# Performance work log

Measured on AMD Instinct MI355X. Metric: run time of the kernel, lower is better.

The kernel has to match this reference:

```python
import jax, jax.numpy as jnp
import numpy as np

B, N, E, I, H = 8, 20000, 320000, 32, 64


def setup_inputs() -> dict:
    key = jax.random.key(0)
    ks = jax.random.split(key, 12)
    s = 0.05
    return {
        "x": jax.random.normal(ks[0], (B, I), jnp.float32),
        "h_prev": jax.random.normal(ks[1], (B, N, H), jnp.float32),
        "src": jax.random.randint(ks[2], (E,), 0, N, jnp.int32),
        "dst": jax.random.randint(ks[3], (E,), 0, N, jnp.int32),
        "w_r_w": jax.random.normal(ks[4], (I, H), jnp.float32) * s,
        "w_r_b": jnp.zeros((H,), jnp.float32),
        "w_z_w": jax.random.normal(ks[5], (I, H), jnp.float32) * s,
        "w_z_b": jnp.zeros((H,), jnp.float32),
        "w_h_w": jax.random.normal(ks[6], (I, H), jnp.float32) * s,
        "w_h_b": jnp.zeros((H,), jnp.float32),
        "gcn_w": jax.random.normal(ks[7], (H, H), jnp.float32) * s,
        "gcn_b": jnp.zeros((H,), jnp.float32),
    }


def _graph_conv(h, src, dst, gcn_w, gcn_b):
    # DGL GraphConv, norm='both': rst = D_in^{-1/2} A (D_out^{-1/2} (H W)) + b
    num_nodes = h.shape[1]
    ones = jnp.ones((src.shape[0],), h.dtype)
    out_deg = jax.ops.segment_sum(ones, src, num_segments=num_nodes)
    in_deg = jax.ops.segment_sum(ones, dst, num_segments=num_nodes)
    out_norm = jax.lax.rsqrt(jnp.clip(out_deg, 1.0))  # [N]
    in_norm = jax.lax.rsqrt(jnp.clip(in_deg, 1.0))    # [N]
    hw = jnp.einsum('bnh,hk->nbk', h, gcn_w)           # [N,B,H] node-major
    feat = hw * out_norm[:, None, None]
    msgs = feat[src]                                   # [E,B,H] gather
    agg = jax.ops.segment_sum(msgs, dst, num_segments=num_nodes)  # [N,B,H]
    agg = agg * in_norm[:, None, None]
    return jnp.swapaxes(agg, 0, 1) + gcn_b             # [B,N,H]


def reference(x, h_prev, src, dst, w_r_w, w_r_b, w_z_w, w_z_b, w_h_w, w_h_b,
              gcn_w, gcn_b):
    # gcn_h is the same module applied to the same h_prev three times in the
    # original -> compute the aggregation once (identical math).
    a = _graph_conv(h_prev, src, dst, gcn_w, gcn_b)    # [B,N,H]
    xr = (x @ w_r_w + w_r_b)[:, None, :]               # [B,1,H] broadcast over nodes
    xz = (x @ w_z_w + w_z_b)[:, None, :]
    xh = (x @ w_h_w + w_h_b)[:, None, :]
    r_t = jax.nn.sigmoid(xr + a)
    z_t = jax.nn.sigmoid(xz + a)
    h_tilde = jnp.tanh(xh + r_t * a)
    h_t = (1.0 - z_t) * h_prev + z_t * h_tilde
    return h_t
```

## Files before the change

kernel.cpp:

```cpp
#include <hip/hip_runtime.h>
#include <hip/hip_bf16.h>
#include <cstdint>

constexpr int B = 8;
constexpr int N = 20000;
constexpr int E = 320000;
constexpr int I = 32;
constexpr int H = 64;
constexpr int BH = B * H;
constexpr int CAP = 64;
constexpr int PAD = 32;

constexpr int GCN_BLOCKS  = 1250;
constexpr int SCAT_BLOCKS = E / 256;

typedef short short8 __attribute__((ext_vector_type(8)));
typedef float f32x4 __attribute__((ext_vector_type(4)));
typedef float f32x2 __attribute__((ext_vector_type(2)));

__device__ __forceinline__ float bf2f(unsigned short u) {
    union { unsigned int i; float f; } c;
    c.i = ((unsigned int)u) << 16;
    return c.f;
}
__device__ __forceinline__ unsigned short f2bf(float f) {
    unsigned int u = __float_as_uint(f);
    u += 0x7fffu + ((u >> 16) & 1u);
    return (unsigned short)(u >> 16);
}
__device__ __forceinline__ float sigmoidf_(float v) {
    return 1.f / (1.f + __expf(-v));
}
__device__ __forceinline__ float tanhf_(float v) {
    return 2.f / (1.f + __expf(-2.f * v)) - 1.f;
}

__global__ __launch_bounds__(256) void fused_pre(
    const float* __restrict__ h_prev, const float* __restrict__ gcn_w,
    const int* __restrict__ src, const int* __restrict__ dst,
    int* __restrict__ cursor, int* __restrict__ out_cnt,
    unsigned short* __restrict__ slots,
    const float* __restrict__ x,
    const float* __restrict__ wr, const float* __restrict__ br,
    const float* __restrict__ wz, const float* __restrict__ bz,
    const float* __restrict__ wh, const float* __restrict__ bh,
    float* __restrict__ xrzh,
    unsigned char* __restrict__ feat)
{
    __shared__ __attribute__((aligned(16))) unsigned short Wt[64 * 72];
    __shared__ __attribute__((aligned(16))) char tbuf[4][1024];
    __shared__ float xs[B * I];

    int bid = blockIdx.x;
    int tid = threadIdx.x;

    if (bid >= GCN_BLOCKS) {
        if (bid < GCN_BLOCKS + SCAT_BLOCKS) {
            int i = (bid - GCN_BLOCKS) * 256 + tid;
            int s = src[i];
            int d = dst[i];
            int pos = atomicAdd(&cursor[d * PAD], 1);
            if (pos < CAP) slots[d * CAP + pos] = (unsigned short)s;
            atomicAdd(&out_cnt[s * PAD], 1);
        } else {
            xs[tid] = x[tid];
            __syncthreads();
            for (int idx = tid; idx < 3 * BH; idx += 256) {
                int mat = idx >> 9;
                int rem = idx & 511;
                int b   = rem >> 6;
                int k   = rem & 63;
                const float* w    = (mat == 0) ? wr : (mat == 1) ? wz : wh;
                const float* bias = (mat == 0) ? br : (mat == 1) ? bz : bh;
                float acc = bias[k];
                #pragma unroll
                for (int i = 0; i < I; ++i)
                    acc = fmaf(xs[b * I + i], w[i * H + k], acc);
                xrzh[idx] = acc;
            }
        }
        return;
    }

    int w    = tid >> 6;
    int lane = tid & 63;
    int r = lane & 15;
    int g = lane >> 4;

    for (int i2 = tid; i2 < H * H; i2 += 256) {
        int hh = i2 >> 6, kk = i2 & 63;
        Wt[kk * 72 + hh] = f2bf(gcn_w[i2]);
    }
    __syncthreads();

    short8 bfrag[2][4];
    #pragma unroll
    for (int kt = 0; kt < 2; ++kt)
        #pragma unroll
        for (int nt = 0; nt < 4; ++nt)
            bfrag[kt][nt] = *(const short8*)&Wt[(nt * 16 + r) * 72 + kt * 32 + g * 8];

    int b = r & 7;
    char* tb8 = tbuf[w];
    int wv = bid * 4 + w;
    for (int np = wv; np < N / 2; np += 4 * GCN_BLOCKS) {
        int node = 2 * np + (r >> 3);
        const float* hp = h_prev + ((size_t)b * N + node) * H + g * 8;
        f32x4 x0 = __builtin_nontemporal_load((const f32x4*)hp);
        f32x4 x1 = __builtin_nontemporal_load((const f32x4*)(hp + 4));
        f32x4 x2 = __builtin_nontemporal_load((const f32x4*)(hp + 32));
        f32x4 x3 = __builtin_nontemporal_load((const f32x4*)(hp + 36));
        short8 a0, a1;
        #pragma unroll
        for (int j = 0; j < 4; ++j) {
            a0[j]     = (short)f2bf(x0[j]);
            a0[j + 4] = (short)f2bf(x1[j]);
            a1[j]     = (short)f2bf(x2[j]);
            a1[j + 4] = (short)f2bf(x3[j]);
        }
        f32x4 acc[4];
        #pragma unroll
        for (int nt = 0; nt < 4; ++nt) { acc[nt][0] = 0.f; acc[nt][1] = 0.f; acc[nt][2] = 0.f; acc[nt][3] = 0.f; }
        #pragma unroll
        for (int nt = 0; nt < 4; ++nt)
            acc[nt] = __builtin_amdgcn_mfma_f32_16x16x32_bf16(a0, bfrag[0][nt], acc[nt], 0, 0, 0);
        #pragma unroll
        for (int nt = 0; nt < 4; ++nt)
            acc[nt] = __builtin_amdgcn_mfma_f32_16x16x32_bf16(a1, bfrag[1][nt], acc[nt], 0, 0, 0);

        #pragma unroll
        for (int nt = 0; nt < 4; ++nt) {
            int v = __builtin_amdgcn_cvt_pk_fp8_f32(acc[nt][0], acc[nt][1], 0, false);
            v = __builtin_amdgcn_cvt_pk_fp8_f32(acc[nt][2], acc[nt][3], v, true);
            int ob = (g >> 1) * 512 + (nt * 16 + r) * 8 + (g & 1) * 4;
            *(int*)&tb8[ob] = v;
        }
        int4 vv = *(const int4*)(tb8 + lane * 16);
        *(int4*)(feat + (size_t)np * 1024 + lane * 16) = vv;
    }
}

__global__ __launch_bounds__(256) void agg_gru(
    const unsigned char* __restrict__ feat,
    const int* __restrict__ in_cnt,
    const int* __restrict__ out_cnt,
    const unsigned short* __restrict__ slots,
    const float* __restrict__ xrzh,
    const float* __restrict__ gcn_b,
    const float* __restrict__ h_prev,
    float* __restrict__ out)
{
    int n    = blockIdx.x * 4 + (threadIdx.x >> 6);
    n = __builtin_amdgcn_readfirstlane(n);
    int lane = threadIdx.x & 63;

    int cnt_raw = in_cnt[n * PAD];
    int cnt = min(cnt_raw, CAP);
    int my_sv = 0;
    if (lane < cnt) {
        int s = (int)__builtin_nontemporal_load(slots + (size_t)n * CAP + lane);
        float on = rsqrtf(fmaxf((float)out_cnt[s * PAD], 1.f));
        my_sv = ((int)f2bf(on) << 16) | s;
    }
    int ru = (cnt + 7) & ~7;

    float acc[8] = {0.f, 0.f, 0.f, 0.f, 0.f, 0.f, 0.f, 0.f};
    for (int i = 0; i < ru; i += 8) {
        #pragma unroll
        for (int u = 0; u < 8; ++u) {
            int sv = __builtin_amdgcn_readlane(my_sv, i + u);
            const uint2* row = (const uint2*)(feat + (size_t)((unsigned)sv & 0xffffu) * 512);
            uint2 v = row[lane];
            float o = __uint_as_float((unsigned)sv & 0xffff0000u);
            f32x2 p01 = __builtin_amdgcn_cvt_pk_f32_fp8((int)v.x, false);
            f32x2 p23 = __builtin_amdgcn_cvt_pk_f32_fp8((int)v.x, true);
            f32x2 p45 = __builtin_amdgcn_cvt_pk_f32_fp8((int)v.y, false);
            f32x2 p67 = __builtin_amdgcn_cvt_pk_f32_fp8((int)v.y, true);
            acc[0] = fmaf(o, p01[0], acc[0]); acc[1] = fmaf(o, p01[1], acc[1]);
            acc[2] = fmaf(o, p23[0], acc[2]); acc[3] = fmaf(o, p23[1], acc[3]);
            acc[4] = fmaf(o, p45[0], acc[4]); acc[5] = fmaf(o, p45[1], acc[5]);
            acc[6] = fmaf(o, p67[0], acc[6]); acc[7] = fmaf(o, p67[1], acc[7]);
        }
    }

    float innorm = rsqrtf(fmaxf((float)cnt_raw, 1.f));
    float gb = gcn_b[lane];
    #pragma unroll
    for (int b = 0; b < 8; ++b) {
        float a  = fmaf(acc[b], innorm, gb);
        float xr = xrzh[b * H + lane];
        float xz = xrzh[BH + b * H + lane];
        float xh = xrzh[2 * BH + b * H + lane];
        float rr = sigmoidf_(xr + a);
        float zz = sigmoidf_(xz + a);
        float tt = tanhf_(xh + rr * a);
        size_t hidx = ((size_t)b * N + n) * H + lane;
        float hp = __builtin_nontemporal_load(h_prev + hidx);
        __builtin_nontemporal_store((1.f - zz) * hp + zz * tt, out + hidx);
    }
}

extern "C" void kernel_launch(void* const* d_in, const int* in_sizes, int n_in,
                              void* d_out, int out_size, void* d_ws, size_t ws_size,
                              hipStream_t stream) {
    const float* x      = (const float*)d_in[0];
    const float* h_prev = (const float*)d_in[1];
    const int*   src    = (const int*)d_in[2];
    const int*   dst    = (const int*)d_in[3];
    const float* w_r_w  = (const float*)d_in[4];
    const float* w_r_b  = (const float*)d_in[5];
    const float* w_z_w  = (const float*)d_in[6];
    const float* w_z_b  = (const float*)d_in[7];
    const float* w_h_w  = (const float*)d_in[8];
    const float* w_h_b  = (const float*)d_in[9];
    const float* gcn_w  = (const float*)d_in[10];
    const float* gcn_b  = (const float*)d_in[11];
    float* out = (float*)d_out;

    char* ws = (char*)d_ws;
    size_t off = 0;
    unsigned char* feat = (unsigned char*)(ws + off); off += (size_t)N * BH;
    off = (off + 255) & ~(size_t)255;
    float* xrzh = (float*)(ws + off);  off += (size_t)3 * BH * sizeof(float);
    off = (off + 255) & ~(size_t)255;
    int* cnts = (int*)(ws + off);
    int* cursor  = cnts;
    int* out_cnt = cnts + N * PAD;     off += (size_t)2 * N * PAD * sizeof(int);
    unsigned short* slots = (unsigned short*)(ws + off);
    off += (size_t)N * CAP * sizeof(unsigned short);

    hipMemsetAsync(cnts, 0, (size_t)2 * N * PAD * sizeof(int), stream);

    fused_pre<<<GCN_BLOCKS + SCAT_BLOCKS + 1, 256, 0, stream>>>(
        h_prev, gcn_w, src, dst, cursor, out_cnt, slots,
        x, w_r_w, w_r_b, w_z_w, w_z_b, w_h_w, w_h_b, xrzh, feat);

    agg_gru<<<N / 4, 256, 0, stream>>>(
        feat, cursor, out_cnt, slots, xrzh, gcn_b, h_prev, out);
}
```

Measured before the change: 85.71 us.

## Split fused pre-kernel into scatter and GEMM kernels, drop counter padding

```diff
diff --git a/kernel.cpp b/kernel.cpp
--- a/kernel.cpp
+++ b/kernel.cpp
@@ -9,10 +9,10 @@
 constexpr int H = 64;
 constexpr int BH = B * H;
 constexpr int CAP = 64;
-constexpr int PAD = 32;
-
-constexpr int GCN_BLOCKS  = 1250;
-constexpr int SCAT_BLOCKS = E / 256;
+
+constexpr int GCN_BLOCKS  = 625;
+constexpr int SCAT_BLOCKS = 320;
+constexpr int SCAT_STRIDE = SCAT_BLOCKS * 256;
 
 typedef short short8 __attribute__((ext_vector_type(8)));
 typedef float f32x4 __attribute__((ext_vector_type(4)));
@@ -35,8 +35,7 @@
     return 2.f / (1.f + __expf(-2.f * v)) - 1.f;
 }
 
-__global__ __launch_bounds__(256) void fused_pre(
-    const float* __restrict__ h_prev, const float* __restrict__ gcn_w,
+__global__ __launch_bounds__(256) void scatter_xw(
     const int* __restrict__ src, const int* __restrict__ dst,
     int* __restrict__ cursor, int* __restrict__ out_cnt,
     unsigned short* __restrict__ slots,
@@ -44,44 +43,57 @@
     const float* __restrict__ wr, const float* __restrict__ br,
     const float* __restrict__ wz, const float* __restrict__ bz,
     const float* __restrict__ wh, const float* __restrict__ bh,
-    float* __restrict__ xrzh,
+    float* __restrict__ xrzh)
+{
+    int bid = blockIdx.x;
+    int tid = threadIdx.x;
+    if (bid == SCAT_BLOCKS) {
+        __shared__ float xs[B * I];
+        xs[tid] = x[tid];
+        __syncthreads();
+        for (int idx = tid; idx < 3 * BH; idx += 256) {
+            int mat = idx >> 9;
+            int rem = idx & 511;
+            int b   = rem >> 6;
+            int k   = rem & 63;
+            const float* w    = (mat == 0) ? wr : (mat == 1) ? wz : wh;
+            const float* bias = (mat == 0) ? br : (mat == 1) ? bz : bh;
+            float acc = bias[k];
+            #pragma unroll
+            for (int i = 0; i < I; ++i)
+                acc = fmaf(xs[b * I + i], w[i * H + k], acc);
+            xrzh[idx] = acc;
+        }
+        return;
+    }
+    int base = bid * 256 + tid;
+    int sv[4], dv[4]; bool ok[4];
+    #pragma unroll
+    for (int u = 0; u < 4; ++u) {
+        int e = base + u * SCAT_STRIDE;
+        ok[u] = (e < E);
+        sv[u] = ok[u] ? src[e] : 0;
+        dv[u] = ok[u] ? dst[e] : 0;
+    }
+    int pos[4];
+    #pragma unroll
+    for (int u = 0; u < 4; ++u)
+        if (ok[u]) pos[u] = atomicAdd(&cursor[dv[u]], 1);
+    #pragma unroll
+    for (int u = 0; u < 4; ++u)
+        if (ok[u]) {
+            if (pos[u] < CAP) slots[dv[u] * CAP + pos[u]] = (unsigned short)sv[u];
+            atomicAdd(&out_cnt[sv[u]], 1);
+        }
+}
+
+__global__ __launch_bounds__(256) void gcn_mm(
+    const float* __restrict__ h_prev, const float* __restrict__ gcn_w,
     unsigned char* __restrict__ feat)
 {
     __shared__ __attribute__((aligned(16))) unsigned short Wt[64 * 72];
     __shared__ __attribute__((aligned(16))) char tbuf[4][1024];
-    __shared__ float xs[B * I];
-
-    int bid = blockIdx.x;
-    int tid = threadIdx.x;
-
-    if (bid >= GCN_BLOCKS) {
-        if (bid < GCN_BLOCKS + SCAT_BLOCKS) {
-            int i = (bid - GCN_BLOCKS) * 256 + tid;
-            int s = src[i];
-            int d = dst[i];
-            int pos = atomicAdd(&cursor[d * PAD], 1);
-            if (pos < CAP) slots[d * CAP + pos] = (unsigned short)s;
-            atomicAdd(&out_cnt[s * PAD], 1);
-        } else {
-            xs[tid] = x[tid];
-            __syncthreads();
-            for (int idx = tid; idx < 3 * BH; idx += 256) {
-                int mat = idx >> 9;
-                int rem = idx & 511;
-                int b   = rem >> 6;
-                int k   = rem & 63;
-                const float* w    = (mat == 0) ? wr : (mat == 1) ? wz : wh;
-                const float* bias = (mat == 0) ? br : (mat == 1) ? bz : bh;
-                float acc = bias[k];
-                #pragma unroll
-                for (int i = 0; i < I; ++i)
-                    acc = fmaf(xs[b * I + i], w[i * H + k], acc);
-                xrzh[idx] = acc;
-            }
-        }
-        return;
-    }
-
+    int tid  = threadIdx.x;
     int w    = tid >> 6;
     int lane = tid & 63;
     int r = lane & 15;
@@ -102,7 +114,7 @@
 
     int b = r & 7;
     char* tb8 = tbuf[w];
-    int wv = bid * 4 + w;
+    int wv = blockIdx.x * 4 + w;
     for (int np = wv; np < N / 2; np += 4 * GCN_BLOCKS) {
         int node = 2 * np + (r >> 3);
         const float* hp = h_prev + ((size_t)b * N + node) * H + g * 8;
@@ -154,20 +166,20 @@
     n = __builtin_amdgcn_readfirstlane(n);
     int lane = threadIdx.x & 63;
 
-    int cnt_raw = in_cnt[n * PAD];
+    int cnt_raw = in_cnt[n];
     int cnt = min(cnt_raw, CAP);
     int my_sv = 0;
     if (lane < cnt) {
         int s = (int)__builtin_nontemporal_load(slots + (size_t)n * CAP + lane);
-        float on = rsqrtf(fmaxf((float)out_cnt[s * PAD], 1.f));
+        float on = rsqrtf(fmaxf((float)out_cnt[s], 1.f));
         my_sv = ((int)f2bf(on) << 16) | s;
     }
-    int ru = (cnt + 7) & ~7;
+    int ru = (cnt + 3) & ~3;
 
     float acc[8] = {0.f, 0.f, 0.f, 0.f, 0.f, 0.f, 0.f, 0.f};
-    for (int i = 0; i < ru; i += 8) {
-        #pragma unroll
-        for (int u = 0; u < 8; ++u) {
+    for (int i = 0; i < ru; i += 4) {
+        #pragma unroll
+        for (int u = 0; u < 4; ++u) {
             int sv = __builtin_amdgcn_readlane(my_sv, i + u);
             const uint2* row = (const uint2*)(feat + (size_t)((unsigned)sv & 0xffffu) * 512);
             uint2 v = row[lane];
@@ -225,15 +237,17 @@
     off = (off + 255) & ~(size_t)255;
     int* cnts = (int*)(ws + off);
     int* cursor  = cnts;
-    int* out_cnt = cnts + N * PAD;     off += (size_t)2 * N * PAD * sizeof(int);
+    int* out_cnt = cnts + N;           off += (size_t)2 * N * sizeof(int);
     unsigned short* slots = (unsigned short*)(ws + off);
     off += (size_t)N * CAP * sizeof(unsigned short);
 
-    hipMemsetAsync(cnts, 0, (size_t)2 * N * PAD * sizeof(int), stream);
-
-    fused_pre<<<GCN_BLOCKS + SCAT_BLOCKS + 1, 256, 0, stream>>>(
-        h_prev, gcn_w, src, dst, cursor, out_cnt, slots,
-        x, w_r_w, w_r_b, w_z_w, w_z_b, w_h_w, w_h_b, xrzh, feat);
+    hipMemsetAsync(cnts, 0, (size_t)2 * N * sizeof(int), stream);
+
+    scatter_xw<<<SCAT_BLOCKS + 1, 256, 0, stream>>>(
+        src, dst, cursor, out_cnt, slots,
+        x, w_r_w, w_r_b, w_z_w, w_z_b, w_h_w, w_h_b, xrzh);
+
+    gcn_mm<<<GCN_BLOCKS, 256, 0, stream>>>(h_prev, gcn_w, feat);
 
     agg_gru<<<N / 4, 256, 0, stream>>>(
         feat, cursor, out_cnt, slots, xrzh, gcn_b, h_prev, out);
```

Result: slower. 94.38 us (+10.1%).
